# Optimization experiments

Measured on AMD Instinct MI355X. Metric: run time of the kernel, lower is better.

## Reference

```python
import jax, jax.numpy as jnp
import numpy as np

B, N, R, T, E, H, FE = 2, 512, 64, 128, 64, 8, 4
D = E // H  # head_dim = 8


def _layernorm(x, g, b):
    m = x.mean(-1, keepdims=True)
    v = ((x - m) ** 2).mean(-1, keepdims=True)
    return (x - m) / jnp.sqrt(v + 1e-5) * g + b


def _sattn(v, k, q, Wv, Wk, Wq, Wo, bo, mask):
    # v,k: (Bk,Nk,T,E); q: (Bq,Nq,T,E) with Bq possibly 1 (broadcast on batch)
    Bk, Nk, Tk, _ = v.shape
    Nq = q.shape[1]
    v = v.reshape(Bk, Nk, Tk, H, D) @ Wv
    k = k.reshape(Bk, Nk, Tk, H, D) @ Wk
    q = q.reshape(q.shape[0], Nq, Tk, H, D) @ Wq
    q = jnp.broadcast_to(q, (Bk, Nq, Tk, H, D))
    energy = jnp.einsum('bqthd,bkthd->bqkth', q, k)  # (B,Nq,Nk,T,H)
    if mask is not None:
        m = mask[None, :, :, None, None]
        energy = energy * m + (-1e8) * (1.0 - m)
    # note: non-standard softmax over the QUERY axis (dim=1), after scale+clamp
    att = jax.nn.softmax(jnp.clip(energy * (float(E) ** -0.5), -5.0, 5.0), axis=1)
    out = jnp.einsum('bqkth,bkthd->bqthd', att, v).reshape(Bk, Nq, Tk, E)
    return out @ Wo + bo, att


def setup_inputs() -> dict:
    rng = jax.random.key(0)
    ks = jax.random.split(rng, 40)
    s = 0.05
    inp = {
        'value': jax.random.normal(ks[0], (B, N, T, E), jnp.float32),
        'key': jax.random.normal(ks[1], (B, N, T, E), jnp.float32),
        'query': jax.random.normal(ks[2], (B, N, T, E), jnp.float32),
        'adj_sr': jax.random.randint(ks[3], (N, R), 0, 2).astype(jnp.int32),
        'adj_r': jax.random.randint(ks[4], (R, R), 0, 2).astype(jnp.int32),
        'D_S': jax.random.normal(ks[5], (N, R), jnp.float32) * s,
        'W_emb': jax.random.normal(ks[6], (R, E), jnp.float32) * s,
        'b_emb': jnp.zeros((E,), jnp.float32),
        'I_param': jax.random.normal(ks[7], (R, 1, E), jnp.float32) * s,
        'g1': jnp.ones((E,), jnp.float32), 'beta1': jnp.zeros((E,), jnp.float32),
        'g2': jnp.ones((E,), jnp.float32), 'beta2': jnp.zeros((E,), jnp.float32),
        'W_ff1': jax.random.normal(ks[8], (E, FE * E), jnp.float32) * s,
        'b_ff1': jnp.zeros((FE * E,), jnp.float32),
        'W_ff2': jax.random.normal(ks[9], (FE * E, E), jnp.float32) * s,
        'b_ff2': jnp.zeros((E,), jnp.float32),
        'W_fs': jax.random.normal(ks[10], (E, E), jnp.float32) * s,
        'b_fs': jnp.zeros((E,), jnp.float32),
    }
    i = 11
    for tag in ('sr', 'rr', 'rs'):
        inp['Wv_' + tag] = jax.random.normal(ks[i + 0], (D, D), jnp.float32) * s
        inp['Wk_' + tag] = jax.random.normal(ks[i + 1], (D, D), jnp.float32) * s
        inp['Wq_' + tag] = jax.random.normal(ks[i + 2], (D, D), jnp.float32) * s
        inp['Wo_' + tag] = jax.random.normal(ks[i + 3], (E, E), jnp.float32) * s
        inp['bo_' + tag] = jnp.zeros((E,), jnp.float32)
        i += 4
    return inp


def reference(value, key, query, adj_sr, adj_r, D_S, W_emb, b_emb, I_param,
              g1, beta1, g2, beta2, W_ff1, b_ff1, W_ff2, b_ff2, W_fs, b_fs,
              Wv_sr, Wk_sr, Wq_sr, Wo_sr, bo_sr,
              Wv_rr, Wk_rr, Wq_rr, Wo_rr, bo_rr,
              Wv_rs, Wk_rs, Wq_rs, Wo_rs, bo_rs):
    m_sr = adj_sr.T.astype(jnp.float32)  # (R,N)
    m_r = adj_r.astype(jnp.float32)      # (R,R)
    ds = D_S @ W_emb + b_emb             # (N,E)
    q = query + ds[None, :, None, :]
    k = key + ds[None, :, None, :]
    v = value
    Iq = jnp.broadcast_to(I_param[None], (1, R, T, E))  # I.repeat(1,1,T,1)
    Hh, asr = _sattn(v, k, Iq, Wv_sr, Wk_sr, Wq_sr, Wo_sr, bo_sr, m_sr)
    Hh, arr = _sattn(Hh, Hh, Hh, Wv_rr, Wk_rr, Wq_rr, Wo_rr, bo_rr, m_r)
    attn, ars = _sattn(Hh, Hh, q, Wv_rs, Wk_rs, Wq_rs, Wo_rs, bo_rs, None)
    x = _layernorm(attn + q, g1, beta1)          # dropout=0.0 -> identity
    ff = jax.nn.relu(x @ W_ff1 + b_ff1) @ W_ff2 + b_ff2
    U = _layernorm(ff + x, g2, beta2)
    out = U @ W_fs + b_fs
    return (out, asr, arr, ars, Hh)
```

## Files before the change

### kernel.cpp

```cpp
#include <hip/hip_runtime.h>
#include <hip/hip_bf16.h>

typedef __hip_bfloat16 bf16;

#define Bc 2
#define Nc 512
#define Rc 64
#define Tc 128
#define Ec 64
#define Hc 8
#define THc 1024
#define FFc 256

__device__ __forceinline__ bf16  f2b(float x){ return __float2bfloat16(x); }
__device__ __forceinline__ float us2f(unsigned short u){
  union { unsigned int i; float f; } c; c.i = ((unsigned int)u) << 16; return c.f;
}
__device__ __forceinline__ float clip5(float x){ return fminf(fmaxf(x, -5.0f), 5.0f); }

__device__ __forceinline__ void wave_sum64x2(float& a, float& b){
#pragma unroll
  for (int o = 32; o > 0; o >>= 1){
    a += __shfl_xor(a, o, 64);
    b += __shfl_xor(b, o, 64);
  }
}
__device__ __forceinline__ void wave_sum64x4(float& a, float& b, float& c, float& d){
#pragma unroll
  for (int o = 32; o > 0; o >>= 1){
    a += __shfl_xor(a, o, 64);
    b += __shfl_xor(b, o, 64);
    c += __shfl_xor(c, o, 64);
    d += __shfl_xor(d, o, 64);
  }
}

__device__ __forceinline__ float rowred16_sum(float v){
  v += __shfl_xor(v, 1, 64);
  v += __shfl_xor(v, 2, 64);
  v += __shfl_xor(v, 4, 64);
  v += __shfl_xor(v, 8, 64);
  return v;
}

__global__ __launch_bounds__(64) void k_prep(
    const float* __restrict__ DS, const float* __restrict__ Wemb,
    const float* __restrict__ bemb, const float* __restrict__ Ip,
    const float* __restrict__ Wq, float* __restrict__ ds, float* __restrict__ qhat)
{
  int bid = blockIdx.x, t = threadIdx.x;
  if (bid < Nc){
    int n = bid, e = t;
    __shared__ float row[Rc];
    row[t] = DS[n*Rc + t];
    __syncthreads();
    float acc = bemb[e];
    for (int r = 0; r < Rc; ++r) acc += row[r] * Wemb[r*Ec + e];
    ds[n*Ec + e] = acc;
  } else {
    int r = bid - Nc;
    __shared__ float irow[Ec];
    irow[t] = Ip[r*Ec + t];
    __syncthreads();
    int h = t >> 3, d = t & 7;
    float acc = 0.0f;
#pragma unroll
    for (int d0 = 0; d0 < 8; ++d0) acc += irow[h*8 + d0] * Wq[d0*8 + d];
    qhat[r*Ec + h*8 + d] = acc;
  }
}

__global__ __launch_bounds__(256) void k_proj_sr(
    const float* __restrict__ key, const float* __restrict__ value,
    const float* __restrict__ ds, const float* __restrict__ Wk,
    const float* __restrict__ Wv, float* __restrict__ khat, float* __restrict__ vhat)
{
  __shared__ float wk[64], wv[64];
  int t = threadIdx.x;
  if (t < 64){ wk[t] = Wk[t]; wv[t] = Wv[t]; }
  __syncthreads();
  int u = blockIdx.x*256 + t;
  int h = u & 7;
  int nt = u >> 3;
  int n = (nt / Tc) % Nc;
  const float* kp = key + (size_t)u*8;
  const float* vp = value + (size_t)u*8;
  const float* dsp = ds + n*Ec + h*8;
  float kin[8], vin[8];
#pragma unroll
  for (int d = 0; d < 8; ++d){ kin[d] = kp[d] + dsp[d]; vin[d] = vp[d]; }
  float* ko = khat + (size_t)u*8;
  float* vo = vhat + (size_t)u*8;
#pragma unroll
  for (int d = 0; d < 8; ++d){
    float ka = 0.0f, va = 0.0f;
#pragma unroll
    for (int d0 = 0; d0 < 8; ++d0){ ka += kin[d0]*wk[d0*8+d]; va += vin[d0]*wv[d0*8+d]; }
    ko[d] = ka; vo[d] = va;
  }
}

__global__ __launch_bounds__(256) void k_asr_write(
    const float* __restrict__ khat, const float* __restrict__ qhat,
    const int* __restrict__ adj_sr, float* __restrict__ o_asr,
    float* __restrict__ rDsr)
{
  __shared__ float ql[4096];
  const float EXPM5 = 0.006737946999085467f;
  int bid = blockIdx.x;
  int b = bid >> 8, np = bid & 255;
  int tid = threadIdx.x;
  int n = np*2 + (tid >> 7);
  int t = tid & 127;
#pragma unroll
  for (int i = 0; i < 16; ++i) ql[i*256 + tid] = qhat[i*256 + tid];
  __syncthreads();
  const float* kp = khat + ((size_t)((b*Nc + n)*Tc + t))*Ec;
  float kr[64];
#pragma unroll
  for (int i = 0; i < 16; ++i) *(float4*)&kr[i*4] = *(const float4*)&kp[i*4];

  float s[8] = {0,0,0,0,0,0,0,0};
  for (int r = 0; r < 64; ++r){
    int m = adj_sr[n*Rc + r];
    if (m){
      const float* qr = &ql[r*64];
#pragma unroll
      for (int h = 0; h < 8; ++h){
        float4 qa = *(const float4*)&qr[h*8];
        float4 qb = *(const float4*)&qr[h*8 + 4];
        float e = qa.x*kr[h*8+0] + qa.y*kr[h*8+1] + qa.z*kr[h*8+2] + qa.w*kr[h*8+3]
                + qb.x*kr[h*8+4] + qb.y*kr[h*8+5] + qb.z*kr[h*8+6] + qb.w*kr[h*8+7];
        s[h] += __expf(clip5(e*0.125f));
      }
    } else {
#pragma unroll
      for (int h = 0; h < 8; ++h) s[h] += EXPM5;
    }
  }
  float rs_[8];
#pragma unroll
  for (int h = 0; h < 8; ++h) rs_[h] = __builtin_amdgcn_rcpf(s[h]);
  {
    size_t dbase = ((size_t)((b*Nc + n)*Tc + t))*8;
    *(float4*)&rDsr[dbase]     = make_float4(rs_[0], rs_[1], rs_[2], rs_[3]);
    *(float4*)&rDsr[dbase + 4] = make_float4(rs_[4], rs_[5], rs_[6], rs_[7]);
  }

  for (int r = 0; r < 64; ++r){
    int m = adj_sr[n*Rc + r];
    float a[8];
    if (m){
      const float* qr = &ql[r*64];
#pragma unroll
      for (int h = 0; h < 8; ++h){
        float4 qa = *(const float4*)&qr[h*8];
        float4 qb = *(const float4*)&qr[h*8 + 4];
        float e = qa.x*kr[h*8+0] + qa.y*kr[h*8+1] + qa.z*kr[h*8+2] + qa.w*kr[h*8+3]
                + qb.x*kr[h*8+4] + qb.y*kr[h*8+5] + qb.z*kr[h*8+6] + qb.w*kr[h*8+7];
        a[h] = __expf(clip5(e*0.125f)) * rs_[h];
      }
    } else {
#pragma unroll
      for (int h = 0; h < 8; ++h) a[h] = EXPM5 * rs_[h];
    }
    size_t ao = ((size_t)((b*Rc + r)*Nc + n))*THc + t*8;
    *(float4*)&o_asr[ao]     = make_float4(a[0], a[1], a[2], a[3]);
    *(float4*)&o_asr[ao + 4] = make_float4(a[4], a[5], a[6], a[7]);
  }
}

__global__ __launch_bounds__(256) void k_attn_sr(
    const float* __restrict__ khat, const float* __restrict__ vhat,
    const float* __restrict__ qhat, const int* __restrict__ adj_sr,
    const float* __restrict__ rD, float* __restrict__ pre)
{
  __shared__ float accs[4][64][8];
  __shared__ float rDl[512];
  int bid = blockIdx.x;
  int b = bid >> 10, th = bid & 1023;
  int t = th >> 3, h = th & 7;
  int tid = threadIdx.x;
  int r = tid & 63, w = tid >> 6;
  rDl[tid]       = rD[((size_t)((b*Nc + tid      )*Tc + t))*8 + h];
  rDl[tid + 256] = rD[((size_t)((b*Nc + tid + 256)*Tc + t))*8 + h];
  float q[8];
#pragma unroll
  for (int d = 0; d < 8; ++d) q[d] = qhat[r*Ec + h*8 + d];
  __syncthreads();
  float acc[8] = {0,0,0,0,0,0,0,0};
  int n0 = w*128;
  for (int n = n0; n < n0 + 128; n += 2){
    size_t goA = ((size_t)((b*Nc + n)*Tc + t))*Ec + h*8;
    size_t goB = goA + (size_t)Tc*Ec;
    const float* kA = khat + goA;
    const float* kB = khat + goB;
    float eA = 0.0f, eB = 0.0f;
#pragma unroll
    for (int d = 0; d < 8; ++d){ eA += q[d]*kA[d]; eB += q[d]*kB[d]; }
    int mA = adj_sr[n*Rc + r], mB = adj_sr[(n+1)*Rc + r];
    eA = mA ? clip5(eA*0.125f) : -5.0f;
    eB = mB ? clip5(eB*0.125f) : -5.0f;
    float aA = __expf(eA) * rDl[n];
    float aB = __expf(eB) * rDl[n+1];
    const float* vA = vhat + goA;
    const float* vB = vhat + goB;
#pragma unroll
    for (int d = 0; d < 8; ++d) acc[d] += aA*vA[d] + aB*vB[d];
  }
#pragma unroll
  for (int d = 0; d < 8; ++d) accs[w][r][d] = acc[d];
  __syncthreads();
  if (w == 0){
    size_t po = ((size_t)((b*Rc + r)*Tc + t))*Ec + h*8;
#pragma unroll
    for (int d = 0; d < 8; ++d)
      pre[po + d] = accs[0][r][d] + accs[1][r][d] + accs[2][r][d] + accs[3][r][d];
  }
}

__global__ __launch_bounds__(256) void k_attn_rr(
    const float* __restrict__ qh, const float* __restrict__ kh,
    const float* __restrict__ vh, const int* __restrict__ adj_r,
    bf16* __restrict__ att_c, float* __restrict__ pre)
{
  __shared__ float accs[4][64][8];
  int bid = blockIdx.x;
  int b = bid >> 10, th = bid & 1023;
  int t = th >> 3, h = th & 7;
  int tid = threadIdx.x;
  int q = tid & 63, w = tid >> 6;
  size_t qo = ((size_t)((b*Rc + q)*Tc + t))*Ec + h*8;
  float qv[8];
#pragma unroll
  for (int d = 0; d < 8; ++d) qv[d] = qh[qo + d];
  float acc[8] = {0,0,0,0,0,0,0,0};
  int k0 = w*16;
  for (int k = k0; k < k0 + 16; k += 2){
    size_t koA = ((size_t)((b*Rc + k)*Tc + t))*Ec + h*8;
    size_t koB = koA + (size_t)Tc*Ec;
    const float* kA = kh + koA;
    const float* kB = kh + koB;
    float eA = 0.0f, eB = 0.0f;
#pragma unroll
    for (int d = 0; d < 8; ++d){ eA += qv[d]*kA[d]; eB += qv[d]*kB[d]; }
    int mA = adj_r[q*Rc + k], mB = adj_r[q*Rc + k + 1];
    eA = mA ? clip5(eA*0.125f) : -5.0f;
    eB = mB ? clip5(eB*0.125f) : -5.0f;
    float pA = __expf(eA), pB = __expf(eB);
    float sA = pA, sB = pB;
    wave_sum64x2(sA, sB);
    float aA = pA/sA, aB = pB/sB;
    size_t ao = ((size_t)(b*Rc + k)*THc + th)*Rc + q;
    att_c[ao] = f2b(aA);
    att_c[ao + (size_t)THc*Rc] = f2b(aB);
    const float* vA = vh + koA;
    const float* vB = vh + koB;
#pragma unroll
    for (int d = 0; d < 8; ++d) acc[d] += aA*vA[d] + aB*vB[d];
  }
#pragma unroll
  for (int d = 0; d < 8; ++d) accs[w][q][d] = acc[d];
  __syncthreads();
  if (w == 0){
#pragma unroll
    for (int d = 0; d < 8; ++d)
      pre[qo + d] = accs[0][q][d] + accs[1][q][d] + accs[2][q][d] + accs[3][q][d];
  }
}

__global__ __launch_bounds__(512) void k_attn_rs(
    const float* __restrict__ query, const float* __restrict__ ds,
    const float* __restrict__ Wq, const float* __restrict__ kh,
    const float* __restrict__ vh, float* __restrict__ rDrs,
    float* __restrict__ pre)
{
  __shared__ float wq[64];
  __shared__ float kl[64][8];
  __shared__ float vl[64][8];
  __shared__ float part[8][64];
  __shared__ float redr[64];
  int bid = blockIdx.x;
  int b = bid >> 10, th = bid & 1023;
  int t = th >> 3, h = th & 7;
  int q = threadIdx.x;
  if (q < 64) wq[q] = Wq[q];
  {
    int kk = q >> 3, d = q & 7;
    size_t o = ((size_t)((b*Rc + kk)*Tc + t))*Ec + h*8 + d;
    kl[kk][d] = kh[o];
    vl[kk][d] = vh[o];
  }
  __syncthreads();
  size_t qro = ((size_t)((b*Nc + q)*Tc + t))*Ec + h*8;
  const float* dsp = ds + q*Ec + h*8;
  float xin[8], qv[8];
#pragma unroll
  for (int d = 0; d < 8; ++d) xin[d] = query[qro + d] + dsp[d];
#pragma unroll
  for (int d = 0; d < 8; ++d){
    float a = 0.0f;
#pragma unroll
    for (int d0 = 0; d0 < 8; ++d0) a += xin[d0]*wq[d0*8 + d];
    qv[d] = a;
  }
  int lane = q & 63, wv = q >> 6;
  for (int k = 0; k < 64; k += 4){
    float s0 = 0.0f, s1 = 0.0f, s2 = 0.0f, s3 = 0.0f;
#pragma unroll
    for (int d = 0; d < 8; ++d){
      s0 += qv[d]*kl[k  ][d];
      s1 += qv[d]*kl[k+1][d];
      s2 += qv[d]*kl[k+2][d];
      s3 += qv[d]*kl[k+3][d];
    }
    s0 = __expf(clip5(s0*0.125f));
    s1 = __expf(clip5(s1*0.125f));
    s2 = __expf(clip5(s2*0.125f));
    s3 = __expf(clip5(s3*0.125f));
    wave_sum64x4(s0, s1, s2, s3);
    if (lane == 0){
      part[wv][k] = s0; part[wv][k+1] = s1; part[wv][k+2] = s2; part[wv][k+3] = s3;
    }
  }
  __syncthreads();
  if (q < 64){
    float s = 0.0f;
#pragma unroll
    for (int w2 = 0; w2 < 8; ++w2) s += part[w2][q];
    float r_ = __builtin_amdgcn_rcpf(s);
    redr[q] = r_;
    rDrs[((size_t)((b*Rc + q)*Tc + t))*8 + h] = r_;
  }
  __syncthreads();
  float acc[8] = {0,0,0,0,0,0,0,0};
  for (int k = 0; k < 64; k += 2){
    float eA = 0.0f, eB = 0.0f;
#pragma unroll
    for (int d = 0; d < 8; ++d){ eA += qv[d]*kl[k][d]; eB += qv[d]*kl[k+1][d]; }
    float aA = __expf(clip5(eA*0.125f)) * redr[k];
    float aB = __expf(clip5(eB*0.125f)) * redr[k+1];
#pragma unroll
    for (int d = 0; d < 8; ++d) acc[d] += aA*vl[k][d] + aB*vl[k+1][d];
  }
#pragma unroll
  for (int d = 0; d < 8; ++d) pre[qro + d] = acc[d];
}

__global__ __launch_bounds__(512) void k_ars_write(
    const float* __restrict__ query, const float* __restrict__ ds,
    const float* __restrict__ Wq, const float* __restrict__ kh,
    const float* __restrict__ rD, float* __restrict__ o_ars)
{
  __shared__ float wq[64];
  int bid = blockIdx.x;
  int tblk = bid & 1; int qg = (bid >> 1) & 63; int b = bid >> 7;
  int tid = threadIdx.x;
  int dt = tid >> 3, h = tid & 7;
  int t = tblk*64 + dt;
  if (tid < 64) wq[tid] = Wq[tid];
  __syncthreads();
  float qv[8][8];
#pragma unroll
  for (int qi = 0; qi < 8; ++qi){
    int q = qg*8 + qi;
    const float* qp = query + ((size_t)((b*Nc + q)*Tc + t))*Ec + h*8;
    const float* dp = ds + q*Ec + h*8;
    float xin[8];
#pragma unroll
    for (int d = 0; d < 8; ++d) xin[d] = qp[d] + dp[d];
#pragma unroll
    for (int d = 0; d < 8; ++d){
      float a = 0.0f;
#pragma unroll
      for (int d0 = 0; d0 < 8; ++d0) a += xin[d0]*wq[d0*8 + d];
      qv[qi][d] = a;
    }
  }
  size_t qbase = ((size_t)(b*Nc + qg*8)*Rc)*THc + t*8 + h;
  for (int k = 0; k < 64; ++k){
    const float* kp = kh + ((size_t)((b*Rc + k)*Tc + t))*Ec + h*8;
    float khr[8];
#pragma unroll
    for (int d = 0; d < 8; ++d) khr[d] = kp[d];
    float rd = rD[((size_t)((b*Rc + k)*Tc + t))*8 + h];
#pragma unroll
    for (int qi = 0; qi < 8; ++qi){
      float e = 0.0f;
#pragma unroll
      for (int d = 0; d < 8; ++d) e += qv[qi][d]*khr[d];
      float a = __expf(clip5(e*0.125f)) * rd;
      o_ars[qbase + (size_t)qi*Rc*THc + (size_t)k*THc] = a;
    }
  }
}

__global__ __launch_bounds__(256) void k_transpose(
    const unsigned short* __restrict__ src, float* __restrict__ dst,
    int W, int C)
{
  __shared__ unsigned short tile[64][66];
  int bid = blockIdx.x;
  int nct = C >> 6;
  int ct = bid % nct; bid /= nct;
  int tht = bid & 15; bid >>= 4;
  int w = bid % W; int b = bid / W;
  int tt = threadIdx.x;
  {
    int cs = tt & 63, i0 = tt >> 6;
    const unsigned short* sb = src + ((size_t)(b*W + w)*THc + tht*64)*C + ct*64;
#pragma unroll
    for (int p = 0; p < 16; ++p){
      int i = i0 + p*4;
      tile[i][cs] = sb[(size_t)i*C + cs];
    }
  }
  __syncthreads();
  {
    int i = tt & 63, c0 = tt >> 6;
#pragma unroll
    for (int p = 0; p < 16; ++p){
      int cs = c0 + p*4;
      int c = ct*64 + cs;
      dst[((size_t)(b*C + c)*W + w)*THc + tht*64 + i] = us2f(tile[i][cs]);
    }
  }
}

__device__ __forceinline__ void gemm64x64(
    const float (* __restrict__ Xs)[68], const float* __restrict__ W,
    int Wld, int r0, int c0, float acc[4][4])
{
#pragma unroll 4
  for (int k = 0; k < 64; k += 4){
    float4 xr0 = *(const float4*)&Xs[r0+0][k];
    float4 xr1 = *(const float4*)&Xs[r0+1][k];
    float4 xr2 = *(const float4*)&Xs[r0+2][k];
    float4 xr3 = *(const float4*)&Xs[r0+3][k];
#pragma unroll
    for (int kk = 0; kk < 4; ++kk){
      float4 w = *(const float4*)&W[(size_t)(k+kk)*Wld + c0];
      float x0 = (&xr0.x)[kk], x1 = (&xr1.x)[kk];
      float x2 = (&xr2.x)[kk], x3 = (&xr3.x)[kk];
      acc[0][0] += x0*w.x; acc[0][1] += x0*w.y; acc[0][2] += x0*w.z; acc[0][3] += x0*w.w;
      acc[1][0] += x1*w.x; acc[1][1] += x1*w.y; acc[1][2] += x1*w.z; acc[1][3] += x1*w.w;
      acc[2][0] += x2*w.x; acc[2][1] += x2*w.y; acc[2][2] += x2*w.z; acc[2][3] += x2*w.w;
      acc[3][0] += x3*w.x; acc[3][1] += x3*w.y; acc[3][2] += x3*w.z; acc[3][3] += x3*w.w;
    }
  }
}

__global__ __launch_bounds__(256) void k_wo(
    const float* __restrict__ pre, const float* __restrict__ Wo,
    const float* __restrict__ bo, float* __restrict__ outf,
    float* __restrict__ outf2)
{
  __shared__ float Xs[64][68];
  int tid = threadIdx.x;
  int cg = tid & 15, rg = tid >> 4;
  int r0 = rg*4, c0 = cg*4;
  int row_base = blockIdx.x * 64;
#pragma unroll
  for (int i = 0; i < 4; ++i)
    *(float4*)&Xs[r0+i][c0] = *(const float4*)&pre[(size_t)(row_base + r0 + i)*64 + c0];
  float4 bo4 = *(const float4*)&bo[c0];
  __syncthreads();
  float acc[4][4];
#pragma unroll
  for (int i = 0; i < 4; ++i){
    acc[i][0] = bo4.x; acc[i][1] = bo4.y; acc[i][2] = bo4.z; acc[i][3] = bo4.w;
  }
  gemm64x64(Xs, Wo, 64, r0, c0, acc);
#pragma unroll
  for (int i = 0; i < 4; ++i){
    float4 v = make_float4(acc[i][0], acc[i][1], acc[i][2], acc[i][3]);
    *(float4*)&outf[(size_t)(row_base + r0 + i)*64 + c0] = v;
    if (outf2) *(float4*)&outf2[(size_t)(row_base + r0 + i)*64 + c0] = v;
  }
}

__global__ __launch_bounds__(256) void k_proj3(
    const float* __restrict__ src, const float* Wq, const float* Wk, const float* Wv,
    float* qh, float* kh, float* vh, int nunits)
{
  __shared__ float wq[64], wk[64], wv[64];
  int t = threadIdx.x;
  if (t < 64){
    wq[t] = Wq ? Wq[t] : 0.0f;
    wk[t] = Wk[t];
    wv[t] = Wv[t];
  }
  __syncthreads();
  int u = blockIdx.x*256 + t;
  if (u >= nunits) return;
  const float* sp = src + (size_t)u*8;
  float xin[8];
#pragma unroll
  for (int d = 0; d < 8; ++d) xin[d] = sp[d];
#pragma unroll
  for (int d = 0; d < 8; ++d){
    float qa = 0.0f, ka = 0.0f, va = 0.0f;
#pragma unroll
    for (int d0 = 0; d0 < 8; ++d0){
      qa += xin[d0]*wq[d0*8 + d];
      ka += xin[d0]*wk[d0*8 + d];
      va += xin[d0]*wv[d0*8 + d];
    }
    if (qh) qh[(size_t)u*8 + d] = qa;
    kh[(size_t)u*8 + d] = ka;
    vh[(size_t)u*8 + d] = va;
  }
}

__device__ __forceinline__ void ln64(
    const float acc[4][4], float4 g, float4 b, float out[4][4])
{
#pragma unroll
  for (int i = 0; i < 4; ++i){
    float s = acc[i][0] + acc[i][1] + acc[i][2] + acc[i][3];
    float m = rowred16_sum(s) * (1.0f/64.0f);
    float d0 = acc[i][0] - m, d1 = acc[i][1] - m, d2 = acc[i][2] - m, d3 = acc[i][3] - m;
    float vv = d0*d0 + d1*d1 + d2*d2 + d3*d3;
    float var = rowred16_sum(vv) * (1.0f/64.0f);
    float rs = rsqrtf(var + 1e-5f);
    out[i][0] = d0*rs*g.x + b.x;
    out[i][1] = d1*rs*g.y + b.y;
    out[i][2] = d2*rs*g.z + b.z;
    out[i][3] = d3*rs*g.w + b.w;
  }
}

__global__ __launch_bounds__(256) void k_tail(
    const float* __restrict__ pre3, const float* __restrict__ query,
    const float* __restrict__ ds,
    const float* __restrict__ Wo, const float* __restrict__ bo,
    const float* __restrict__ g1, const float* __restrict__ be1,
    const float* __restrict__ W1, const float* __restrict__ b1,
    const float* __restrict__ W2, const float* __restrict__ b2,
    const float* __restrict__ g2, const float* __restrict__ be2,
    const float* __restrict__ Wfs, const float* __restrict__ bfs,
    float* __restrict__ outp)
{
  __shared__ float Xs[64][68];
  __shared__ float Hs[64][68];
  int tid = threadIdx.x;
  int cg = tid & 15, rg = tid >> 4;
  int r0 = rg*4, c0 = cg*4;
  int row_base = blockIdx.x * 64;
  int n = (row_base >> 7) & (Nc - 1);

#pragma unroll
  for (int i = 0; i < 4; ++i){
    float4 t = *(const float4*)&pre3[(size_t)(row_base + r0 + i)*64 + c0];
    *(float4*)&Xs[r0+i][c0] = t;
  }

  float4 bo4  = *(const float4*)&bo[c0];
  float4 ds4  = *(const float4*)&ds[n*64 + c0];
  float4 g14  = *(const float4*)&g1[c0];
  float4 be14 = *(const float4*)&be1[c0];
  float4 b24  = *(const float4*)&b2[c0];
  float4 g24  = *(const float4*)&g2[c0];
  float4 be24 = *(const float4*)&be2[c0];
  float4 bfs4 = *(const float4*)&bfs[c0];
  __syncthreads();

  float acc[4][4];
#pragma unroll
  for (int i = 0; i < 4; ++i){
    acc[i][0] = bo4.x; acc[i][1] = bo4.y; acc[i][2] = bo4.z; acc[i][3] = bo4.w;
  }
  gemm64x64(Xs, Wo, 64, r0, c0, acc);
#pragma unroll
  for (int i = 0; i < 4; ++i){
    float4 qv = *(const float4*)&query[(size_t)(row_base + r0 + i)*64 + c0];
    acc[i][0] += qv.x + ds4.x;
    acc[i][1] += qv.y + ds4.y;
    acc[i][2] += qv.z + ds4.z;
    acc[i][3] += qv.w + ds4.w;
  }
  float xt[4][4];
  ln64(acc, g14, be14, xt);
  __syncthreads();
#pragma unroll
  for (int i = 0; i < 4; ++i)
    *(float4*)&Xs[r0+i][c0] = make_float4(xt[i][0], xt[i][1], xt[i][2], xt[i][3]);
  __syncthreads();

  float ff[4][4];
#pragma unroll
  for (int i = 0; i < 4; ++i){
    ff[i][0] = b24.x; ff[i][1] = b24.y; ff[i][2] = b24.z; ff[i][3] = b24.w;
  }
  for (int p = 0; p < 4; ++p){
    float4 b14 = *(const float4*)&b1[p*64 + c0];
    float h[4][4];
#pragma unroll
    for (int i = 0; i < 4; ++i){
      h[i][0] = b14.x; h[i][1] = b14.y; h[i][2] = b14.z; h[i][3] = b14.w;
    }
    gemm64x64(Xs, W1 + p*64, 256, r0, c0, h);
#pragma unroll
    for (int i = 0; i < 4; ++i){
      h[i][0] = fmaxf(h[i][0], 0.0f); h[i][1] = fmaxf(h[i][1], 0.0f);
      h[i][2] = fmaxf(h[i][2], 0.0f); h[i][3] = fmaxf(h[i][3], 0.0f);
    }
    __syncthreads();
#pragma unroll
    for (int i = 0; i < 4; ++i)
      *(float4*)&Hs[r0+i][c0] = make_float4(h[i][0], h[i][1], h[i][2], h[i][3]);
    __syncthreads();
    gemm64x64(Hs, W2 + (size_t)p*64*64, 64, r0, c0, ff);
  }

#pragma unroll
  for (int i = 0; i < 4; ++i){
    float4 xv = *(const float4*)&Xs[r0+i][c0];
    ff[i][0] += xv.x; ff[i][1] += xv.y; ff[i][2] += xv.z; ff[i][3] += xv.w;
  }
  float U[4][4];
  ln64(ff, g24, be24, U);
  __syncthreads();
#pragma unroll
  for (int i = 0; i < 4; ++i)
    *(float4*)&Hs[r0+i][c0] = make_float4(U[i][0], U[i][1], U[i][2], U[i][3]);
  __syncthreads();

  float o[4][4];
#pragma unroll
  for (int i = 0; i < 4; ++i){
    o[i][0] = bfs4.x; o[i][1] = bfs4.y; o[i][2] = bfs4.z; o[i][3] = bfs4.w;
  }
  gemm64x64(Hs, Wfs, 64, r0, c0, o);
#pragma unroll
  for (int i = 0; i < 4; ++i)
    *(float4*)&outp[(size_t)(row_base + r0 + i)*64 + c0] =
        make_float4(o[i][0], o[i][1], o[i][2], o[i][3]);
}

extern "C" void kernel_launch(void* const* d_in, const int* in_sizes, int n_in,
                              void* d_out, int out_size, void* d_ws, size_t ws_size,
                              hipStream_t stream)
{
  const float* value = (const float*)d_in[0];
  const float* key   = (const float*)d_in[1];
  const float* query = (const float*)d_in[2];
  const int*  adj_sr = (const int*)d_in[3];
  const int*  adj_r  = (const int*)d_in[4];
  const float* D_S   = (const float*)d_in[5];
  const float* W_emb = (const float*)d_in[6];
  const float* b_emb = (const float*)d_in[7];
  const float* I_par = (const float*)d_in[8];
  const float* g1    = (const float*)d_in[9];
  const float* be1   = (const float*)d_in[10];
  const float* g2    = (const float*)d_in[11];
  const float* be2   = (const float*)d_in[12];
  const float* W_ff1 = (const float*)d_in[13];
  const float* b_ff1 = (const float*)d_in[14];
  const float* W_ff2 = (const float*)d_in[15];
  const float* b_ff2 = (const float*)d_in[16];
  const float* W_fs  = (const float*)d_in[17];
  const float* b_fs  = (const float*)d_in[18];
  const float* Wv_sr = (const float*)d_in[19];
  const float* Wk_sr = (const float*)d_in[20];
  const float* Wq_sr = (const float*)d_in[21];
  const float* Wo_sr = (const float*)d_in[22];
  const float* bo_sr = (const float*)d_in[23];
  const float* Wv_rr = (const float*)d_in[24];
  const float* Wk_rr = (const float*)d_in[25];
  const float* Wq_rr = (const float*)d_in[26];
  const float* Wo_rr = (const float*)d_in[27];
  const float* bo_rr = (const float*)d_in[28];
  const float* Wv_rs = (const float*)d_in[29];
  const float* Wk_rs = (const float*)d_in[30];
  const float* Wq_rs = (const float*)d_in[31];
  const float* Wo_rs = (const float*)d_in[32];
  const float* bo_rs = (const float*)d_in[33];

  float* outp  = (float*)d_out;
  float* o_out = outp;
  float* o_asr = outp + 8388608;
  float* o_arr = outp + 75497472;
  float* o_ars = outp + 83886080;
  float* o_hh  = outp + 150994944;

  float* wsf = (float*)d_ws;
  float* ws_ds   = wsf;
  float* ws_qsr  = wsf + 32768;
  bf16*  ws_att  = (bf16*)(wsf + 36864);
  float* ws_rDsr = wsf + 36864;
  float* pool    = wsf + 36864 + 33554432;
  float* ws_ksr  = pool;
  float* ws_vsr  = pool + 8388608;
  float* ws_pre1 = pool + 16777216;
  float* ws_hh1  = pool + 17825792;
  float* ws_qrr  = pool;
  float* ws_krr  = pool + 1048576;
  float* ws_vrr  = pool + 2097152;
  float* ws_pre2 = pool + 3145728;
  float* ws_hh2  = pool + 4194304;
  float* ws_krs  = pool + 5242880;
  float* ws_vrs  = pool + 6291456;
  float* ws_pre3 = pool + 7340032;
  float* ws_rDrs = pool + 15728640;

  k_prep<<<576, 64, 0, stream>>>(D_S, W_emb, b_emb, I_par, Wq_sr, ws_ds, ws_qsr);
  k_proj_sr<<<4096, 256, 0, stream>>>(key, value, ws_ds, Wk_sr, Wv_sr, ws_ksr, ws_vsr);
  k_asr_write<<<512, 256, 0, stream>>>(ws_ksr, ws_qsr, adj_sr, o_asr, ws_rDsr);
  k_attn_sr<<<2048, 256, 0, stream>>>(ws_ksr, ws_vsr, ws_qsr, adj_sr,
                                      ws_rDsr, ws_pre1);
  k_wo<<<256, 256, 0, stream>>>(ws_pre1, Wo_sr, bo_sr, ws_hh1, (float*)nullptr);

  k_proj3<<<512, 256, 0, stream>>>(ws_hh1, Wq_rr, Wk_rr, Wv_rr,
                                   ws_qrr, ws_krr, ws_vrr, 131072);
  k_attn_rr<<<2048, 256, 0, stream>>>(ws_qrr, ws_krr, ws_vrr, adj_r, ws_att, ws_pre2);
  k_transpose<<<2048, 256, 0, stream>>>((const unsigned short*)ws_att, o_arr, 64, 64);
  k_wo<<<256, 256, 0, stream>>>(ws_pre2, Wo_rr, bo_rr, ws_hh2, o_hh);

  k_proj3<<<512, 256, 0, stream>>>(ws_hh2, (const float*)nullptr, Wk_rs, Wv_rs,
                                   (float*)nullptr, ws_krs, ws_vrs, 131072);
  k_attn_rs<<<2048, 512, 0, stream>>>(query, ws_ds, Wq_rs, ws_krs, ws_vrs,
                                      ws_rDrs, ws_pre3);
  k_ars_write<<<256, 512, 0, stream>>>(query, ws_ds, Wq_rs, ws_krs,
                                       ws_rDrs, o_ars);

  k_tail<<<2048, 256, 0, stream>>>(ws_pre3, query, ws_ds, Wo_rs, bo_rs,
                                   g1, be1, W_ff1, b_ff1, W_ff2, b_ff2,
                                   g2, be2, W_fs, b_fs, o_out);
}
```

Baseline: 816.2 us.

## Recompute rr attention weights directly in output layout and fuse Wo with projections

The rr attention kernel no longer writes a bf16 attention tensor that a separate kernel transposes into the output. It now stores only per-key reciprocal softmax denominators, and a new kernel recomputes the weights and writes them straight into the final layout. The Wo output GEMM and the following per-head Q/K/V projection are also fused into one kernel, which keeps the intermediate Hh in shared memory and drops two launches plus their global round trips. The cost is recomputing the q·k dot products, and the attention weights are now written in fp32 instead of being rounded through bf16.

```diff
diff --git a/kernel.cpp b/kernel.cpp
--- a/kernel.cpp
+++ b/kernel.cpp
@@ -1,7 +1,5 @@
 #include <hip/hip_runtime.h>
 #include <hip/hip_bf16.h>
-
-typedef __hip_bfloat16 bf16;
 
 #define Bc 2
 #define Nc 512
@@ -12,10 +10,6 @@
 #define THc 1024
 #define FFc 256
 
-__device__ __forceinline__ bf16  f2b(float x){ return __float2bfloat16(x); }
-__device__ __forceinline__ float us2f(unsigned short u){
-  union { unsigned int i; float f; } c; c.i = ((unsigned int)u) << 16; return c.f;
-}
 __device__ __forceinline__ float clip5(float x){ return fminf(fmaxf(x, -5.0f), 5.0f); }
 
 __device__ __forceinline__ void wave_sum64x2(float& a, float& b){
@@ -222,7 +216,7 @@
 __global__ __launch_bounds__(256) void k_attn_rr(
     const float* __restrict__ qh, const float* __restrict__ kh,
     const float* __restrict__ vh, const int* __restrict__ adj_r,
-    bf16* __restrict__ att_c, float* __restrict__ pre)
+    float* __restrict__ rDrr, float* __restrict__ pre)
 {
   __shared__ float accs[4][64][8];
   int bid = blockIdx.x;
@@ -250,10 +244,12 @@
     float pA = __expf(eA), pB = __expf(eB);
     float sA = pA, sB = pB;
     wave_sum64x2(sA, sB);
-    float aA = pA/sA, aB = pB/sB;
-    size_t ao = ((size_t)(b*Rc + k)*THc + th)*Rc + q;
-    att_c[ao] = f2b(aA);
-    att_c[ao + (size_t)THc*Rc] = f2b(aB);
+    float rA = __builtin_amdgcn_rcpf(sA), rB = __builtin_amdgcn_rcpf(sB);
+    if (q == 0){
+      rDrr[((size_t)((b*Rc + k  )*Tc + t))*8 + h] = rA;
+      rDrr[((size_t)((b*Rc + k+1)*Tc + t))*8 + h] = rB;
+    }
+    float aA = pA*rA, aB = pB*rB;
     const float* vA = vh + koA;
     const float* vB = vh + koB;
 #pragma unroll
@@ -266,6 +262,39 @@
 #pragma unroll
     for (int d = 0; d < 8; ++d)
       pre[qo + d] = accs[0][q][d] + accs[1][q][d] + accs[2][q][d] + accs[3][q][d];
+  }
+}
+
+__global__ __launch_bounds__(512) void k_arr_write(
+    const float* __restrict__ qh, const float* __restrict__ kh,
+    const int* __restrict__ adj_r, const float* __restrict__ rD,
+    float* __restrict__ o_arr)
+{
+  const float EXPM5 = 0.006737946999085467f;
+  int bid = blockIdx.x;
+  int tblk = bid & 1; int q = (bid >> 1) & 63; int b = bid >> 7;
+  int tid = threadIdx.x;
+  int dt = tid >> 3, h = tid & 7;
+  int t = tblk*64 + dt;
+  float qv[8];
+  const float* qp = qh + ((size_t)((b*Rc + q)*Tc + t))*Ec + h*8;
+#pragma unroll
+  for (int d = 0; d < 8; ++d) qv[d] = qp[d];
+  const int* am = adj_r + q*Rc;
+  size_t obase = ((size_t)(b*Rc + q)*Rc)*THc + (size_t)t*8 + h;
+  for (int k = 0; k < 64; ++k){
+    float rd = rD[((size_t)((b*Rc + k)*Tc + t))*8 + h];
+    float a;
+    if (am[k]){
+      const float* kp = kh + ((size_t)((b*Rc + k)*Tc + t))*Ec + h*8;
+      float e = 0.0f;
+#pragma unroll
+      for (int d = 0; d < 8; ++d) e += qv[d]*kp[d];
+      a = __expf(clip5(e*0.125f)) * rd;
+    } else {
+      a = EXPM5 * rd;
+    }
+    o_arr[obase + (size_t)k*THc] = a;
   }
 }
 
@@ -395,38 +424,6 @@
   }
 }
 
-__global__ __launch_bounds__(256) void k_transpose(
-    const unsigned short* __restrict__ src, float* __restrict__ dst,
-    int W, int C)
-{
-  __shared__ unsigned short tile[64][66];
-  int bid = blockIdx.x;
-  int nct = C >> 6;
-  int ct = bid % nct; bid /= nct;
-  int tht = bid & 15; bid >>= 4;
-  int w = bid % W; int b = bid / W;
-  int tt = threadIdx.x;
-  {
-    int cs = tt & 63, i0 = tt >> 6;
-    const unsigned short* sb = src + ((size_t)(b*W + w)*THc + tht*64)*C + ct*64;
-#pragma unroll
-    for (int p = 0; p < 16; ++p){
-      int i = i0 + p*4;
-      tile[i][cs] = sb[(size_t)i*C + cs];
-    }
-  }
-  __syncthreads();
-  {
-    int i = tt & 63, c0 = tt >> 6;
-#pragma unroll
-    for (int p = 0; p < 16; ++p){
-      int cs = c0 + p*4;
-      int c = ct*64 + cs;
-      dst[((size_t)(b*C + c)*W + w)*THc + tht*64 + i] = us2f(tile[i][cs]);
-    }
-  }
-}
-
 __device__ __forceinline__ void gemm64x64(
     const float (* __restrict__ Xs)[68], const float* __restrict__ W,
     int Wld, int r0, int c0, float acc[4][4])
@@ -450,12 +447,14 @@
   }
 }
 
-__global__ __launch_bounds__(256) void k_wo(
+__global__ __launch_bounds__(256) void k_wo_proj3(
     const float* __restrict__ pre, const float* __restrict__ Wo,
-    const float* __restrict__ bo, float* __restrict__ outf,
-    float* __restrict__ outf2)
+    const float* __restrict__ bo, const float* Wq,
+    const float* __restrict__ Wk, const float* __restrict__ Wv,
+    float* o2, float* qh, float* __restrict__ kh, float* __restrict__ vh)
 {
   __shared__ float Xs[64][68];
+  __shared__ float wqs[64], wks[64], wvs[64];
   int tid = threadIdx.x;
   int cg = tid & 15, rg = tid >> 4;
   int r0 = rg*4, c0 = cg*4;
@@ -463,6 +462,7 @@
 #pragma unroll
   for (int i = 0; i < 4; ++i)
     *(float4*)&Xs[r0+i][c0] = *(const float4*)&pre[(size_t)(row_base + r0 + i)*64 + c0];
+  if (tid < 64){ wqs[tid] = Wq ? Wq[tid] : 0.0f; wks[tid] = Wk[tid]; wvs[tid] = Wv[tid]; }
   float4 bo4 = *(const float4*)&bo[c0];
   __syncthreads();
   float acc[4][4];
@@ -471,44 +471,42 @@
     acc[i][0] = bo4.x; acc[i][1] = bo4.y; acc[i][2] = bo4.z; acc[i][3] = bo4.w;
   }
   gemm64x64(Xs, Wo, 64, r0, c0, acc);
+  __syncthreads();
 #pragma unroll
   for (int i = 0; i < 4; ++i){
     float4 v = make_float4(acc[i][0], acc[i][1], acc[i][2], acc[i][3]);
-    *(float4*)&outf[(size_t)(row_base + r0 + i)*64 + c0] = v;
-    if (outf2) *(float4*)&outf2[(size_t)(row_base + r0 + i)*64 + c0] = v;
-  }
-}
-
-__global__ __launch_bounds__(256) void k_proj3(
-    const float* __restrict__ src, const float* Wq, const float* Wk, const float* Wv,
-    float* qh, float* kh, float* vh, int nunits)
-{
-  __shared__ float wq[64], wk[64], wv[64];
-  int t = threadIdx.x;
-  if (t < 64){
-    wq[t] = Wq ? Wq[t] : 0.0f;
-    wk[t] = Wk[t];
-    wv[t] = Wv[t];
-  }
-  __syncthreads();
-  int u = blockIdx.x*256 + t;
-  if (u >= nunits) return;
-  const float* sp = src + (size_t)u*8;
-  float xin[8];
-#pragma unroll
-  for (int d = 0; d < 8; ++d) xin[d] = sp[d];
-#pragma unroll
-  for (int d = 0; d < 8; ++d){
-    float qa = 0.0f, ka = 0.0f, va = 0.0f;
-#pragma unroll
-    for (int d0 = 0; d0 < 8; ++d0){
-      qa += xin[d0]*wq[d0*8 + d];
-      ka += xin[d0]*wk[d0*8 + d];
-      va += xin[d0]*wv[d0*8 + d];
-    }
-    if (qh) qh[(size_t)u*8 + d] = qa;
-    kh[(size_t)u*8 + d] = ka;
-    vh[(size_t)u*8 + d] = va;
+    *(float4*)&Xs[r0+i][c0] = v;
+    if (o2) *(float4*)&o2[(size_t)(row_base + r0 + i)*64 + c0] = v;
+  }
+  __syncthreads();
+#pragma unroll
+  for (int uu = 0; uu < 2; ++uu){
+    int u = tid + uu*256;
+    int row = u >> 3, hh = u & 7;
+    float xr[8];
+#pragma unroll
+    for (int d = 0; d < 8; ++d) xr[d] = Xs[row][hh*8 + d];
+    float qa[8], ka[8], va[8];
+#pragma unroll
+    for (int d = 0; d < 8; ++d){
+      float qs = 0.0f, ks = 0.0f, vs = 0.0f;
+#pragma unroll
+      for (int d0 = 0; d0 < 8; ++d0){
+        qs += xr[d0]*wqs[d0*8 + d];
+        ks += xr[d0]*wks[d0*8 + d];
+        vs += xr[d0]*wvs[d0*8 + d];
+      }
+      qa[d] = qs; ka[d] = ks; va[d] = vs;
+    }
+    size_t base = (size_t)(row_base + row)*64 + hh*8;
+    if (qh){
+      *(float4*)&qh[base]     = make_float4(qa[0], qa[1], qa[2], qa[3]);
+      *(float4*)&qh[base + 4] = make_float4(qa[4], qa[5], qa[6], qa[7]);
+    }
+    *(float4*)&kh[base]     = make_float4(ka[0], ka[1], ka[2], ka[3]);
+    *(float4*)&kh[base + 4] = make_float4(ka[4], ka[5], ka[6], ka[7]);
+    *(float4*)&vh[base]     = make_float4(va[0], va[1], va[2], va[3]);
+    *(float4*)&vh[base + 4] = make_float4(va[4], va[5], va[6], va[7]);
   }
 }
 
@@ -687,18 +685,16 @@
   float* wsf = (float*)d_ws;
   float* ws_ds   = wsf;
   float* ws_qsr  = wsf + 32768;
-  bf16*  ws_att  = (bf16*)(wsf + 36864);
   float* ws_rDsr = wsf + 36864;
   float* pool    = wsf + 36864 + 33554432;
   float* ws_ksr  = pool;
   float* ws_vsr  = pool + 8388608;
   float* ws_pre1 = pool + 16777216;
-  float* ws_hh1  = pool + 17825792;
   float* ws_qrr  = pool;
   float* ws_krr  = pool + 1048576;
   float* ws_vrr  = pool + 2097152;
   float* ws_pre2 = pool + 3145728;
-  float* ws_hh2  = pool + 4194304;
+  float* ws_rDrr = pool + 4194304;
   float* ws_krs  = pool + 5242880;
   float* ws_vrs  = pool + 6291456;
   float* ws_pre3 = pool + 7340032;
@@ -709,16 +705,17 @@
   k_asr_write<<<512, 256, 0, stream>>>(ws_ksr, ws_qsr, adj_sr, o_asr, ws_rDsr);
   k_attn_sr<<<2048, 256, 0, stream>>>(ws_ksr, ws_vsr, ws_qsr, adj_sr,
                                       ws_rDsr, ws_pre1);
-  k_wo<<<256, 256, 0, stream>>>(ws_pre1, Wo_sr, bo_sr, ws_hh1, (float*)nullptr);
-
-  k_proj3<<<512, 256, 0, stream>>>(ws_hh1, Wq_rr, Wk_rr, Wv_rr,
-                                   ws_qrr, ws_krr, ws_vrr, 131072);
-  k_attn_rr<<<2048, 256, 0, stream>>>(ws_qrr, ws_krr, ws_vrr, adj_r, ws_att, ws_pre2);
-  k_transpose<<<2048, 256, 0, stream>>>((const unsigned short*)ws_att, o_arr, 64, 64);
-  k_wo<<<256, 256, 0, stream>>>(ws_pre2, Wo_rr, bo_rr, ws_hh2, o_hh);
-
-  k_proj3<<<512, 256, 0, stream>>>(ws_hh2, (const float*)nullptr, Wk_rs, Wv_rs,
-                                   (float*)nullptr, ws_krs, ws_vrs, 131072);
+  k_wo_proj3<<<256, 256, 0, stream>>>(ws_pre1, Wo_sr, bo_sr,
+                                      Wq_rr, Wk_rr, Wv_rr,
+                                      (float*)nullptr, ws_qrr, ws_krr, ws_vrr);
+
+  k_attn_rr<<<2048, 256, 0, stream>>>(ws_qrr, ws_krr, ws_vrr, adj_r,
+                                      ws_rDrr, ws_pre2);
+  k_arr_write<<<256, 512, 0, stream>>>(ws_qrr, ws_krr, adj_r, ws_rDrr, o_arr);
+  k_wo_proj3<<<256, 256, 0, stream>>>(ws_pre2, Wo_rr, bo_rr,
+                                      (const float*)nullptr, Wk_rs, Wv_rs,
+                                      o_hh, (float*)nullptr, ws_krs, ws_vrs);
+
   k_attn_rs<<<2048, 512, 0, stream>>>(query, ws_ds, Wq_rs, ws_krs, ws_vrs,
                                       ws_rDrs, ws_pre3);
   k_ars_write<<<256, 512, 0, stream>>>(query, ws_ds, Wq_rs, ws_krs,
```

Result: no change. 818.4 us, median of 2 (+0.3%).
